# Performance work log

Hardware: AMD Instinct MI355X
Metric: run time of the kernel (lower is better)

## Reference

```python
import jax, jax.numpy as jnp
import numpy as np
import math

D_MODEL = 2048
H = 16
Q_LORA = 1536
KV_LORA = 512
DN = 128   # qk_nope_head_dim
DR = 64    # qk_rope_head_dim
DV = 128   # v_head_dim
B, S = 2, 2048
EPS = 1e-5


def layernorm(x, g, b):
    mu = jnp.mean(x, axis=-1, keepdims=True)
    var = jnp.mean(jnp.square(x - mu), axis=-1, keepdims=True)
    return (x - mu) * jax.lax.rsqrt(var + EPS) * g + b


def rope_cos_sin(position_ids, dim):
    inv_freq = 1.0 / (10000.0 ** (jnp.arange(0, dim, 2, dtype=jnp.float32) / dim))
    ang = position_ids.astype(jnp.float32)[:, None] * inv_freq[None, :]  # [S, dim/2]
    return jnp.cos(ang), jnp.sin(ang)


def apply_rope(x, cos, sin):
    # x: [..., S, ..., dim]; cos/sin broadcastable [..., S, ..., dim/2]
    x1, x2 = jnp.split(x, 2, axis=-1)
    return jnp.concatenate([x1 * cos - x2 * sin, x1 * sin + x2 * cos], axis=-1)


def setup_inputs() -> dict:
    key = jax.random.key(0)
    ks = jax.random.split(key, 8)
    sc = 0.02
    return {
        "hidden_states": jax.random.normal(ks[0], (B, S, D_MODEL), jnp.float32),
        "w_qa": jax.random.normal(ks[1], (Q_LORA, D_MODEL), jnp.float32) * sc,
        "ln_qa_g": jnp.ones((Q_LORA,), jnp.float32),
        "ln_qa_b": jnp.zeros((Q_LORA,), jnp.float32),
        "w_qb": jax.random.normal(ks[2], (H * DN, Q_LORA), jnp.float32) * sc,
        "w_qrope": jax.random.normal(ks[3], (H * DR, Q_LORA), jnp.float32) * sc,
        "w_kva": jax.random.normal(ks[4], (KV_LORA + DR, D_MODEL), jnp.float32) * sc,
        "ln_kva_g": jnp.ones((KV_LORA,), jnp.float32),
        "ln_kva_b": jnp.zeros((KV_LORA,), jnp.float32),
        "w_kvb": jax.random.normal(ks[5], (H * (DN + DV), KV_LORA), jnp.float32) * sc,
        "w_o": jax.random.normal(ks[6], (D_MODEL, H * DV), jnp.float32) * sc,
        "position_ids": jnp.arange(S, dtype=jnp.int32),
    }


def reference(hidden_states, w_qa, ln_qa_g, ln_qa_b, w_qb, w_qrope,
              w_kva, ln_kva_g, ln_kva_b, w_kvb, w_o, position_ids):
    bsz, seq_len, _ = hidden_states.shape

    # --- Q path (low-rank) ---
    q_latent = layernorm(hidden_states @ w_qa.T, ln_qa_g, ln_qa_b)        # [B,S,Q_LORA]
    q_nope = (q_latent @ w_qb.T).reshape(bsz, seq_len, H, DN)             # [B,S,H,DN]
    q_rope = (q_latent @ w_qrope.T).reshape(bsz, seq_len, H, DR)          # [B,S,H,DR]

    # --- absorb k up-projection into q ---
    k_up = w_kvb[: H * DN].reshape(H, DN, KV_LORA)
    v_up = w_kvb[H * DN:].reshape(H, DV, KV_LORA)
    q_abs = jnp.einsum('bshd,hdr->bshr', q_nope, k_up)                    # [B,S,H,R]

    # --- KV latent path ---
    kv_mixed = hidden_states @ w_kva.T                                    # [B,S,R+DR]
    kv_latent = layernorm(kv_mixed[..., :KV_LORA], ln_kva_g, ln_kva_b)    # [B,S,R]
    k_rope = kv_mixed[..., KV_LORA:]                                      # [B,S,DR]

    # --- RoPE ---
    cos, sin = rope_cos_sin(position_ids, DR)                             # [S,DR/2]
    q_rope = apply_rope(q_rope, cos[None, :, None, :], sin[None, :, None, :])
    k_rope = apply_rope(k_rope, cos[None, :, :], sin[None, :, :])

    # --- attention over latent channel (keys shared across heads) ---
    q_full = jnp.concatenate([q_abs, q_rope], axis=-1)                    # [B,S,H,R+DR]
    k_full = jnp.concatenate([kv_latent, k_rope], axis=-1)                # [B,S,R+DR]
    scale = 1.0 / math.sqrt(DN + DR)
    scores = jnp.einsum('bqhc,bkc->bhqk', q_full, k_full) * scale
    probs = jax.nn.softmax(scores, axis=-1)
    attn = jnp.einsum('bhqk,bkr->bhqr', probs, kv_latent)                 # [B,H,S,R]

    # --- absorbed v up-projection + output ---
    attn_v = jnp.einsum('bhqr,hvr->bqhv', attn, v_up)                     # [B,S,H,DV]
    attn_v = attn_v.reshape(bsz, seq_len, H * DV)
    return attn_v @ w_o.T                                                 # [B,S,D_MODEL]
```

## Files before the change

kernel.cpp:

```cpp
#include <hip/hip_runtime.h>
#include <math.h>

#define D_MODEL 2048
#define NH 16
#define Q_LORA 1536
#define KV_LORA 512
#define DN 128
#define DR 64
#define DV 128
#define BB 2
#define SS 2048
#define NROWS (BB*SS)
#define LN_EPS 1e-5f

typedef __attribute__((ext_vector_type(8))) short short8;
typedef __attribute__((ext_vector_type(4))) short short4v;
typedef __attribute__((ext_vector_type(4))) float f32x4;

__device__ __forceinline__ ushort f2bf(float f) {
    unsigned int u = __float_as_uint(f);
    u = u + 0x7fffu + ((u >> 16) & 1u);
    return (ushort)(u >> 16);
}

#if __has_builtin(__builtin_amdgcn_mfma_f32_16x16x16bf16_1k)
__device__ __forceinline__ f32x4 mfma16(short4v a, short4v b, f32x4 c) {
    return __builtin_amdgcn_mfma_f32_16x16x16bf16_1k(a, b, c, 0, 0, 0);
}
#elif __has_builtin(__builtin_amdgcn_mfma_f32_16x16x16_bf16)
__device__ __forceinline__ f32x4 mfma16(short4v a, short4v b, f32x4 c) {
    return __builtin_amdgcn_mfma_f32_16x16x16_bf16(a, b, c, 0, 0, 0);
}
#else
__device__ __forceinline__ f32x4 mfma16(short4v a, short4v b, f32x4 c) {
    asm volatile("v_mfma_f32_16x16x16_bf16 %0, %1, %2, %0"
                 : "+v"(c) : "v"(a), "v"(b));
    return c;
}
#endif

__device__ __forceinline__ void cv4(const float* __restrict__ s,
                                    ushort* __restrict__ d, long i) {
    float4 v = ((const float4*)s)[i];
    ushort4 o;
    o.x = f2bf(v.x); o.y = f2bf(v.y); o.z = f2bf(v.z); o.w = f2bf(v.w);
    ((ushort4*)d)[i] = o;
}

__global__ __launch_bounds__(256)
void cvt_all(const float* __restrict__ hs,     const float* __restrict__ w_qa,
             const float* __restrict__ w_qb,   const float* __restrict__ w_qrope,
             const float* __restrict__ w_kvb,  const float* __restrict__ w_kva,
             ushort* __restrict__ hs_bf,       ushort* __restrict__ w_qa_bf,
             ushort* __restrict__ w_qb_bf,     ushort* __restrict__ w_qrope_bf,
             ushort* __restrict__ w_kvb_bf,    ushort* __restrict__ w_kva_bf)
{
    long i = (long)blockIdx.x * 256 + threadIdx.x;
    if (i < 2097152) { cv4(hs, hs_bf, i); return; }
    i -= 2097152;
    if (i < 786432) { cv4(w_qa, w_qa_bf, i); return; }
    i -= 786432;
    if (i < 786432) { cv4(w_qb, w_qb_bf, i); return; }
    i -= 786432;
    if (i < 393216) { cv4(w_qrope, w_qrope_bf, i); return; }
    i -= 393216;
    if (i < 524288) { cv4(w_kvb, w_kvb_bf, i); return; }
    i -= 524288;
    if (i >= 327680) return;
    long e = i * 4;
    int row = (int)(e >> 11), col = (int)(e & 2047);
    ushort4 o;
    if (row < 576) {
        float4 v = *(const float4*)(w_kva + (long)row * 2048 + col);
        o.x = f2bf(v.x); o.y = f2bf(v.y); o.z = f2bf(v.z); o.w = f2bf(v.w);
    } else { o.x = 0; o.y = 0; o.z = 0; o.w = 0; }
    *(ushort4*)(w_kva_bf + (long)row * 2048 + col) = o;
}

__global__ __launch_bounds__(256)
void cvt_bf16(const float* __restrict__ in, ushort* __restrict__ out, long n4)
{
    long i = (long)blockIdx.x * 256 + threadIdx.x;
    if (i >= n4) return;
    cv4(in, out, i);
}

#define GLL16(g, l) \
    __builtin_amdgcn_global_load_lds((const __attribute__((address_space(1))) void*)(g), \
                                     (__attribute__((address_space(3))) void*)(l), 16, 0, 0)

__device__ __forceinline__ void gemm_core(const ushort* __restrict__ A,
    const ushort* __restrict__ Bp, ushort* As, ushort* Bs,
    int K, int lda, int ldb, int m0, int n0, int tid, f32x4 acc[4][4])
{
    int l = tid & 63, w = tid >> 6;
    int l15 = l & 15, quad = l >> 4;
    int wm = (w >> 1) * 64, wn = (w & 1) * 64;
    int ob = tid * 16;
    int row = ob >> 6, colb = ob & 63;
    const char* ga0 = (const char*)(A  + (long)(m0 + row) * lda)      + colb;
    const char* ga1 = (const char*)(A  + (long)(m0 + row + 64) * lda) + colb;
    const char* gb0 = (const char*)(Bp + (long)(n0 + row) * ldb)      + colb;
    const char* gb1 = (const char*)(Bp + (long)(n0 + row + 64) * ldb) + colb;
    ushort* la0 = As + tid * 8;
    ushort* la1 = As + 2048 + tid * 8;
    ushort* lb0 = Bs + tid * 8;
    ushort* lb1 = Bs + 2048 + tid * 8;

    for (int k0 = 0; k0 < K; k0 += 32) {
        GLL16(ga0, la0); GLL16(ga1, la1);
        GLL16(gb0, lb0); GLL16(gb1, lb1);
        ga0 += 64; ga1 += 64; gb0 += 64; gb1 += 64;
        __syncthreads();
        short8 af[4], bf[4];
        #pragma unroll
        for (int i = 0; i < 4; ++i)
            af[i] = *(const short8*)(As + (wm + i * 16 + l15) * 32 + quad * 8);
        #pragma unroll
        for (int j = 0; j < 4; ++j)
            bf[j] = *(const short8*)(Bs + (wn + j * 16 + l15) * 32 + quad * 8);
        #pragma unroll
        for (int i = 0; i < 4; ++i)
            #pragma unroll
            for (int j = 0; j < 4; ++j)
                acc[i][j] = __builtin_amdgcn_mfma_f32_16x16x32_bf16(
                    af[i], bf[j], acc[i][j], 0, 0, 0);
        __syncthreads();
    }
}

__global__ __launch_bounds__(256)
void gemm_f32out(const ushort* __restrict__ A, const ushort* __restrict__ B,
                 float* __restrict__ C, int K, int lda, int ldb, int ldc)
{
    __shared__ __align__(16) ushort As[128 * 32];
    __shared__ __align__(16) ushort Bs[128 * 32];
    int tid = threadIdx.x;
    int m0 = blockIdx.y * 128, n0 = blockIdx.x * 128;
    f32x4 acc[4][4] = {};
    gemm_core(A, B, As, Bs, K, lda, ldb, m0, n0, tid, acc);
    int l = tid & 63, w = tid >> 6;
    int l15 = l & 15, quad = l >> 4;
    int wm = (w >> 1) * 64, wn = (w & 1) * 64;
    #pragma unroll
    for (int i = 0; i < 4; ++i)
        #pragma unroll
        for (int j = 0; j < 4; ++j)
            #pragma unroll
            for (int r = 0; r < 4; ++r) {
                long gm = m0 + wm + i * 16 + quad * 4 + r;
                long gn = n0 + wn + j * 16 + l15;
                C[gm * ldc + gn] = acc[i][j][r];
            }
}

__global__ __launch_bounds__(256)
void gemm_dual(const ushort* __restrict__ A, const ushort* __restrict__ Bqa,
               const ushort* __restrict__ Bkva, float* __restrict__ Cq,
               float* __restrict__ Ckv)
{
    __shared__ __align__(16) ushort As[128 * 32];
    __shared__ __align__(16) ushort Bs[128 * 32];
    int tid = threadIdx.x;
    int bx = blockIdx.x;
    int m0 = blockIdx.y * 128;
    const ushort* Bp; float* C; int ldc, n0;
    if (bx < 12) { n0 = bx * 128;        Bp = Bqa  + (long)n0 * 2048; C = Cq;  ldc = 1536; }
    else         { n0 = (bx - 12) * 128; Bp = Bkva + (long)n0 * 2048; C = Ckv; ldc = 640; }
    f32x4 acc[4][4] = {};
    gemm_core(A, Bp, As, Bs, D_MODEL, D_MODEL, D_MODEL, m0, 0, tid, acc);
    int l = tid & 63, w = tid >> 6;
    int l15 = l & 15, quad = l >> 4;
    int wm = (w >> 1) * 64, wn = (w & 1) * 64;
    #pragma unroll
    for (int i = 0; i < 4; ++i)
        #pragma unroll
        for (int j = 0; j < 4; ++j)
            #pragma unroll
            for (int r = 0; r < 4; ++r) {
                long gm = m0 + wm + i * 16 + quad * 4 + r;
                long gn = n0 + wn + j * 16 + l15;
                C[gm * ldc + gn] = acc[i][j][r];
            }
}

__global__ __launch_bounds__(256)
void gemm_q23(const ushort* __restrict__ A, const ushort* __restrict__ Bqb,
              const ushort* __restrict__ Bqr, ushort* __restrict__ qfull,
              const float2* __restrict__ tab)
{
    __shared__ __align__(16) ushort As[128 * 32];
    __shared__ __align__(16) ushort Bs[128 * 32];
    int tid = threadIdx.x;
    int m0 = blockIdx.y * 128, n0 = blockIdx.x * 128;
    const ushort* Bp = (n0 < 2048) ? Bqb + (long)n0 * Q_LORA
                                   : Bqr + (long)(n0 - 2048) * Q_LORA;
    f32x4 acc[4][4] = {};
    gemm_core(A, Bp, As, Bs, Q_LORA, Q_LORA, Q_LORA, m0, 0, tid, acc);
    int l = tid & 63, w = tid >> 6;
    int l15 = l & 15, quad = l >> 4;
    int wm = (w >> 1) * 64, wn = (w & 1) * 64;
    if (n0 < 2048) {
        int head = n0 >> 7;
        #pragma unroll
        for (int i = 0; i < 4; ++i)
            #pragma unroll
            for (int j = 0; j < 4; ++j)
                #pragma unroll
                for (int r = 0; r < 4; ++r) {
                    long gm = m0 + wm + i * 16 + quad * 4 + r;
                    int c = wn + j * 16 + l15;
                    qfull[(gm * NH + head) * 192 + c] = f2bf(acc[i][j][r]);
                }
    } else {
        int nb = n0 - 2048;
        int head = (nb + wn) >> 6;
        #pragma unroll
        for (int i = 0; i < 4; ++i)
            #pragma unroll
            for (int j = 0; j < 2; ++j)
                #pragma unroll
                for (int r = 0; r < 4; ++r) {
                    long gm = m0 + wm + i * 16 + quad * 4 + r;
                    int ir = j * 16 + l15;
                    int s = (int)(gm & (SS - 1));
                    float2 cs = tab[s * 32 + ir];
                    float x1 = acc[i][j][r], x2 = acc[i][j + 2][r];
                    ushort* op = qfull + (gm * NH + head) * 192 + 128;
                    op[ir]      = f2bf(x1 * cs.x - x2 * cs.y);
                    op[ir + 32] = f2bf(x1 * cs.y + x2 * cs.x);
                }
    }
}

__global__ __launch_bounds__(256)
void gemm_kv56(const ushort* __restrict__ A, const ushort* __restrict__ B,
               ushort* __restrict__ kfull, ushort* __restrict__ vt)
{
    __shared__ __align__(16) ushort As[128 * 32];
    __shared__ __align__(16) ushort Bs[128 * 32];
    int tid = threadIdx.x;
    int m0 = blockIdx.y * 128, n0 = blockIdx.x * 128;
    const ushort* Bp = B + (long)n0 * KV_LORA;
    f32x4 acc[4][4] = {};
    gemm_core(A, Bp, As, Bs, KV_LORA, KV_LORA, KV_LORA, m0, 0, tid, acc);
    int l = tid & 63, w = tid >> 6;
    int l15 = l & 15, quad = l >> 4;
    int wm = (w >> 1) * 64, wn = (w & 1) * 64;
    if (n0 < 2048) {
        int head = n0 >> 7;
        #pragma unroll
        for (int i = 0; i < 4; ++i)
            #pragma unroll
            for (int j = 0; j < 4; ++j)
                #pragma unroll
                for (int r = 0; r < 4; ++r) {
                    long gm = m0 + wm + i * 16 + quad * 4 + r;
                    int c = wn + j * 16 + l15;
                    kfull[(gm * NH + head) * 192 + c] = f2bf(acc[i][j][r]);
                }
    } else {
        int head = (n0 >> 7) - 16;
        #pragma unroll
        for (int i = 0; i < 4; ++i)
            #pragma unroll
            for (int j = 0; j < 4; ++j) {
                long gm0 = m0 + wm + i * 16 + quad * 4;
                int c = wn + j * 16 + l15;
                ushort4 p;
                p.x = f2bf(acc[i][j][0]); p.y = f2bf(acc[i][j][1]);
                p.z = f2bf(acc[i][j][2]); p.w = f2bf(acc[i][j][3]);
                *(ushort4*)(vt + (long)head * 128 * 4096 + (long)c * 4096 + gm0) = p;
            }
    }
}

__global__ __launch_bounds__(256)
void ln_rows_bf(const float* __restrict__ in, ushort* __restrict__ out,
                const float* __restrict__ g, const float* __restrict__ b,
                int n, int ld_in, int ld_out)
{
    long rowi = blockIdx.x;
    const float* x = in + rowi * ld_in;
    ushort* y = out + rowi * ld_out;
    int tid = threadIdx.x;
    float s = 0.f, ss = 0.f;
    for (int i = tid; i < n; i += 256) { float v = x[i]; s += v; ss += v * v; }
    #pragma unroll
    for (int off = 32; off > 0; off >>= 1) {
        s  += __shfl_xor(s, off);
        ss += __shfl_xor(ss, off);
    }
    __shared__ float sred[4], ssred[4];
    int wid = tid >> 6, lane = tid & 63;
    if (lane == 0) { sred[wid] = s; ssred[wid] = ss; }
    __syncthreads();
    s  = sred[0] + sred[1] + sred[2] + sred[3];
    ss = ssred[0] + ssred[1] + ssred[2] + ssred[3];
    float mu  = s / n;
    float var = ss / n - mu * mu;
    float r = 1.0f / sqrtf(var + LN_EPS);
    for (int i = tid; i < n; i += 256)
        y[i] = f2bf((x[i] - mu) * r * g[i] + b[i]);
}

__global__ __launch_bounds__(256)
void rope_tab_k(const int* __restrict__ pos, float2* __restrict__ tab)
{
    int idx = blockIdx.x * 256 + threadIdx.x;
    if (idx >= SS * 32) return;
    int i = idx & 31;
    int s = idx >> 5;
    double ang = (double)pos[s] * exp(-(double)i * 0.28782313662425572);
    float2 cs;
    cs.x = (float)cos(ang);
    cs.y = (float)sin(ang);
    tab[idx] = cs;
}

__global__ __launch_bounds__(256)
void rope_k(const float* __restrict__ kvm, ushort* __restrict__ kfull,
            const float2* __restrict__ tab)
{
    long idx = (long)blockIdx.x * 256 + threadIdx.x;
    if (idx >= (long)NROWS * 32) return;
    int i = (int)(idx & 31);
    long rowi = idx >> 5;
    int s = (int)(rowi & (SS - 1));
    float2 cs = tab[s * 32 + i];
    float c = cs.x, sn = cs.y;
    const float* p = kvm + rowi * 640 + 512;
    float x1 = p[i], x2 = p[i + 32];
    ushort v1 = f2bf(x1 * c - x2 * sn);
    ushort v2 = f2bf(x1 * sn + x2 * c);
    ushort* o = kfull + rowi * NH * 192 + 128;
    #pragma unroll
    for (int h = 0; h < NH; ++h) {
        o[h * 192 + i]      = v1;
        o[h * 192 + i + 32] = v2;
    }
}

#define FSCALE 0.07216878364870322f

__global__ __launch_bounds__(512, 4)
void flash_mfma(const ushort* __restrict__ qf, const ushort* __restrict__ kf,
                const ushort* __restrict__ vt, ushort* __restrict__ attnv)
{
    __shared__ __align__(16) ushort Ks[64 * 192];
    __shared__ __align__(16) ushort Vs[128 * 64];
    int tid = threadIdx.x;
    int w = tid >> 6, l = tid & 63, l15 = l & 15, quad = l >> 4;
    int bh = blockIdx.x;
    int b = bh >> 4, h = bh & 15;
    int q0 = blockIdx.y * 128;

    const ushort* qp = qf + ((long)(b * SS + q0 + 16 * w + l15) * NH + h) * 192 + quad * 8;
    short8 aq[6];
    #pragma unroll
    for (int kk = 0; kk < 6; ++kk) aq[kk] = *(const short8*)(qp + kk * 32);

    f32x4 o[8] = {};
    float lsum = 0.f;
    float mrow = -INFINITY;

    const ushort* kbase = kf + ((long)(b * SS) * NH + h) * 192;
    const ushort* vbase = vt + (long)h * 128 * 4096 + (long)b * SS;

    int r0k = tid >> 3, subk = tid & 7;
    int v0  = tid >> 2, subv = tid & 3;
    const ushort* kgp = kbase + (long)r0k * (NH * 192);
    const ushort* vgp = vbase + (long)v0 * 4096;

    short8 pk[3], pv[2];
    #pragma unroll
    for (int it = 0; it < 3; ++it)
        pk[it] = *(const short8*)(kgp + (subk + 8 * it) * 8);
    #pragma unroll
    for (int it = 0; it < 2; ++it)
        pv[it] = *(const short8*)(vgp + (subv + 4 * it) * 8);

    int ksw = r0k & 7, vsw = v0 & 7;

    for (int k0 = 0; k0 < SS; k0 += 64) {
        __syncthreads();
        #pragma unroll
        for (int it = 0; it < 3; ++it)
            *(short8*)&Ks[r0k * 192 + ((subk + 8 * it) ^ ksw) * 8] = pk[it];
        #pragma unroll
        for (int it = 0; it < 2; ++it)
            *(short8*)&Vs[v0 * 64 + ((subv + 4 * it) ^ vsw) * 8] = pv[it];
        __syncthreads();
        if (k0 + 64 < SS) {
            const ushort* kg = kgp + (long)(k0 + 64) * (NH * 192);
            const ushort* vg = vgp + (k0 + 64);
            #pragma unroll
            for (int it = 0; it < 3; ++it)
                pk[it] = *(const short8*)(kg + (subk + 8 * it) * 8);
            #pragma unroll
            for (int it = 0; it < 2; ++it)
                pv[it] = *(const short8*)(vg + (subv + 4 * it) * 8);
        }

        f32x4 sc[4] = {};
        #pragma unroll
        for (int kk = 0; kk < 6; ++kk) {
            #pragma unroll
            for (int j = 0; j < 4; ++j) {
                int krow = j * 16 + l15;
                short8 kfr = *(const short8*)&Ks[krow * 192 + (((kk * 4 + quad) ^ (krow & 7))) * 8];
                sc[j] = __builtin_amdgcn_mfma_f32_16x16x32_bf16(kfr, aq[kk], sc[j], 0, 0, 0);
            }
        }

        float rmax = fmaxf(
            fmaxf(fmaxf(fmaxf(sc[0][0], sc[0][1]), fmaxf(sc[0][2], sc[0][3])),
                  fmaxf(fmaxf(sc[1][0], sc[1][1]), fmaxf(sc[1][2], sc[1][3]))),
            fmaxf(fmaxf(fmaxf(sc[2][0], sc[2][1]), fmaxf(sc[2][2], sc[2][3])),
                  fmaxf(fmaxf(sc[3][0], sc[3][1]), fmaxf(sc[3][2], sc[3][3]))));
        rmax = fmaxf(rmax, __shfl_xor(rmax, 16));
        rmax = fmaxf(rmax, __shfl_xor(rmax, 32));
        float pmax = rmax * FSCALE;

        if (__any(pmax > mrow + 8.0f)) {
            float mnew = fmaxf(mrow, pmax);
            float alpha = __expf(mrow - mnew);
            mrow = mnew;
            lsum *= alpha;
            float a0 = __shfl(alpha, quad * 4 + 0);
            float a1 = __shfl(alpha, quad * 4 + 1);
            float a2 = __shfl(alpha, quad * 4 + 2);
            float a3 = __shfl(alpha, quad * 4 + 3);
            #pragma unroll
            for (int v8 = 0; v8 < 8; ++v8) {
                o[v8][0] *= a0; o[v8][1] *= a1;
                o[v8][2] *= a2; o[v8][3] *= a3;
            }
        }

        float tsum = 0.f;
        #pragma unroll
        for (int j = 0; j < 4; ++j) {
            float p0 = __expf(fmaf(sc[j][0], FSCALE, -mrow));
            float p1 = __expf(fmaf(sc[j][1], FSCALE, -mrow));
            float p2 = __expf(fmaf(sc[j][2], FSCALE, -mrow));
            float p3 = __expf(fmaf(sc[j][3], FSCALE, -mrow));
            tsum += (p0 + p1) + (p2 + p3);
            short4v pf;
            pf[0] = (short)f2bf(p0); pf[1] = (short)f2bf(p1);
            pf[2] = (short)f2bf(p2); pf[3] = (short)f2bf(p3);
            #pragma unroll
            for (int v8 = 0; v8 < 8; ++v8) {
                int vrow = v8 * 16 + l15;
                int chunk = (2 * j + (quad >> 1)) ^ (vrow & 7);
                short4v bv = *(const short4v*)&Vs[vrow * 64 + chunk * 8 + 4 * (quad & 1)];
                o[v8] = mfma16(pf, bv, o[v8]);
            }
        }
        tsum += __shfl_xor(tsum, 16);
        tsum += __shfl_xor(tsum, 32);
        lsum += tsum;
    }

    #pragma unroll
    for (int r = 0; r < 4; ++r) {
        float Lq = __shfl(lsum, quad * 4 + r);
        float inv = 1.0f / Lq;
        long rowi = (long)(b * SS) + q0 + 16 * w + quad * 4 + r;
        ushort* op = attnv + (rowi * NH + h) * 128;
        #pragma unroll
        for (int v8 = 0; v8 < 8; ++v8)
            op[v8 * 16 + l15] = f2bf(o[v8][r] * inv);
    }
}


extern "C" void kernel_launch(void* const* d_in, const int* in_sizes, int n_in,
                              void* d_out, int out_size, void* d_ws, size_t ws_size,
                              hipStream_t stream) {
    const float* hs       = (const float*)d_in[0];
    const float* w_qa     = (const float*)d_in[1];
    const float* ln_qa_g  = (const float*)d_in[2];
    const float* ln_qa_b  = (const float*)d_in[3];
    const float* w_qb     = (const float*)d_in[4];
    const float* w_qrope  = (const float*)d_in[5];
    const float* w_kva    = (const float*)d_in[6];
    const float* ln_kva_g = (const float*)d_in[7];
    const float* ln_kva_b = (const float*)d_in[8];
    const float* w_kvb    = (const float*)d_in[9];
    const float* w_o      = (const float*)d_in[10];
    const int*   pos      = (const int*)d_in[11];
    float* out = (float*)d_out;

    char* W = (char*)d_ws;
    ushort* hs_bf     = (ushort*)(W + 0);
    ushort* w_o_bf    = (ushort*)(W + 0);
    ushort* w_qa_bf   = (ushort*)(W + 16777216);
    ushort* w_qb_bf   = (ushort*)(W + 23068672);
    ushort* w_qrope_bf= (ushort*)(W + 29360128);
    ushort* w_kva_bf  = (ushort*)(W + 32505856);
    ushort* w_kvb_bf  = (ushort*)(W + 35127296);
    float*  q_lat_f   = (float*)(W + 39321600);
    ushort* q_lat_bf  = (ushort*)(W + 64487424);
    float*  kv_mix    = (float*)(W + 77070336);
    ushort* kv_lat_bf = (ushort*)(W + 87556096);
    ushort* q_full    = (ushort*)(W + 91750400);
    ushort* k_full    = (ushort*)(W + 116916224);
    ushort* v_exp_t   = (ushort*)(W + 142082048);
    ushort* attnv_bf  = (ushort*)(W + 158859264);
    float2* rope_tab  = (float2*)(W + 158859264);

    dim3 blk(256);

    rope_tab_k<<<dim3(256), blk, 0, stream>>>(pos, rope_tab);
    cvt_all<<<dim3(19200), blk, 0, stream>>>(
        hs, w_qa, w_qb, w_qrope, w_kvb, w_kva,
        hs_bf, w_qa_bf, w_qb_bf, w_qrope_bf, w_kvb_bf, w_kva_bf);
    gemm_dual<<<dim3(17, 32), blk, 0, stream>>>(
        hs_bf, w_qa_bf, w_kva_bf, q_lat_f, kv_mix);
    cvt_bf16<<<dim3(4096), blk, 0, stream>>>(w_o, w_o_bf, 1048576);
    ln_rows_bf<<<dim3(NROWS), blk, 0, stream>>>(
        q_lat_f, q_lat_bf, ln_qa_g, ln_qa_b, Q_LORA, Q_LORA, Q_LORA);
    ln_rows_bf<<<dim3(NROWS), blk, 0, stream>>>(
        kv_mix, kv_lat_bf, ln_kva_g, ln_kva_b, KV_LORA, 640, KV_LORA);
    rope_k<<<dim3(512), blk, 0, stream>>>(kv_mix, k_full, rope_tab);
    gemm_q23<<<dim3(24, 32), blk, 0, stream>>>(
        q_lat_bf, w_qb_bf, w_qrope_bf, q_full, rope_tab);
    gemm_kv56<<<dim3(32, 32), blk, 0, stream>>>(
        kv_lat_bf, w_kvb_bf, k_full, v_exp_t);
    flash_mfma<<<dim3(BB * NH, SS / 128), dim3(512), 0, stream>>>(
        q_full, k_full, v_exp_t, attnv_bf);
    gemm_f32out<<<dim3(16, 32), blk, 0, stream>>>(
        attnv_bf, w_o_bf, out, NH * DV, NH * DV, NH * DV, D_MODEL);
}
```

Baseline: 529.8 us.

## Use 16x16x32 MFMA for PV via LDS-staged P and MFMA-computed row sums

Probabilities are now written to an LDS buffer and reread in the A-operand layout, so the PV product uses 16x16x32 bf16 MFMAs instead of 16x16x16. The softmax denominator comes from an extra MFMA against a block of ones appended to the V tile, which drops the per-tile shuffle reductions and summation. s_setprio brackets around the MFMA sections are meant to favour matrix issue. In exchange each tile adds LDS traffic for P, uses more shared memory, and computes the row sum from bf16-rounded probabilities.

```diff
diff --git a/kernel.cpp b/kernel.cpp
--- a/kernel.cpp
+++ b/kernel.cpp
@@ -14,7 +14,6 @@
 #define LN_EPS 1e-5f
 
 typedef __attribute__((ext_vector_type(8))) short short8;
-typedef __attribute__((ext_vector_type(4))) short short4v;
 typedef __attribute__((ext_vector_type(4))) float f32x4;
 
 __device__ __forceinline__ ushort f2bf(float f) {
@@ -22,22 +21,6 @@
     u = u + 0x7fffu + ((u >> 16) & 1u);
     return (ushort)(u >> 16);
 }
-
-#if __has_builtin(__builtin_amdgcn_mfma_f32_16x16x16bf16_1k)
-__device__ __forceinline__ f32x4 mfma16(short4v a, short4v b, f32x4 c) {
-    return __builtin_amdgcn_mfma_f32_16x16x16bf16_1k(a, b, c, 0, 0, 0);
-}
-#elif __has_builtin(__builtin_amdgcn_mfma_f32_16x16x16_bf16)
-__device__ __forceinline__ f32x4 mfma16(short4v a, short4v b, f32x4 c) {
-    return __builtin_amdgcn_mfma_f32_16x16x16_bf16(a, b, c, 0, 0, 0);
-}
-#else
-__device__ __forceinline__ f32x4 mfma16(short4v a, short4v b, f32x4 c) {
-    asm volatile("v_mfma_f32_16x16x16_bf16 %0, %1, %2, %0"
-                 : "+v"(c) : "v"(a), "v"(b));
-    return c;
-}
-#endif
 
 __device__ __forceinline__ void cv4(const float* __restrict__ s,
                                     ushort* __restrict__ d, long i) {
@@ -348,20 +331,29 @@
                 const ushort* __restrict__ vt, ushort* __restrict__ attnv)
 {
     __shared__ __align__(16) ushort Ks[64 * 192];
-    __shared__ __align__(16) ushort Vs[128 * 64];
+    __shared__ __align__(16) ushort Vs[144 * 64];
+    __shared__ __align__(16) ushort Ps[128 * 72];
     int tid = threadIdx.x;
     int w = tid >> 6, l = tid & 63, l15 = l & 15, quad = l >> 4;
     int bh = blockIdx.x;
     int b = bh >> 4, h = bh & 15;
     int q0 = blockIdx.y * 128;
 
+    {
+        int e = 8192 + tid * 2;
+        ushort2 iv;
+        iv.x = (e     < 8256) ? (ushort)0x3F80 : (ushort)0;
+        iv.y = (e + 1 < 8256) ? (ushort)0x3F80 : (ushort)0;
+        *(ushort2*)&Vs[e] = iv;
+    }
+
     const ushort* qp = qf + ((long)(b * SS + q0 + 16 * w + l15) * NH + h) * 192 + quad * 8;
     short8 aq[6];
     #pragma unroll
     for (int kk = 0; kk < 6; ++kk) aq[kk] = *(const short8*)(qp + kk * 32);
 
     f32x4 o[8] = {};
-    float lsum = 0.f;
+    f32x4 osum = {};
     float mrow = -INFINITY;
 
     const ushort* kbase = kf + ((long)(b * SS) * NH + h) * 192;
@@ -403,6 +395,7 @@
         }
 
         f32x4 sc[4] = {};
+        __builtin_amdgcn_s_setprio(1);
         #pragma unroll
         for (int kk = 0; kk < 6; ++kk) {
             #pragma unroll
@@ -412,6 +405,7 @@
                 sc[j] = __builtin_amdgcn_mfma_f32_16x16x32_bf16(kfr, aq[kk], sc[j], 0, 0, 0);
             }
         }
+        __builtin_amdgcn_s_setprio(0);
 
         float rmax = fmaxf(
             fmaxf(fmaxf(fmaxf(sc[0][0], sc[0][1]), fmaxf(sc[0][2], sc[0][3])),
@@ -426,7 +420,6 @@
             float mnew = fmaxf(mrow, pmax);
             float alpha = __expf(mrow - mnew);
             mrow = mnew;
-            lsum *= alpha;
             float a0 = __shfl(alpha, quad * 4 + 0);
             float a1 = __shfl(alpha, quad * 4 + 1);
             float a2 = __shfl(alpha, quad * 4 + 2);
@@ -436,36 +429,45 @@
                 o[v8][0] *= a0; o[v8][1] *= a1;
                 o[v8][2] *= a2; o[v8][3] *= a3;
             }
+            osum[0] *= a0; osum[1] *= a1; osum[2] *= a2; osum[3] *= a3;
         }
 
-        float tsum = 0.f;
+        int prow = (16 * w + l15) * 72 + quad * 4;
         #pragma unroll
         for (int j = 0; j < 4; ++j) {
             float p0 = __expf(fmaf(sc[j][0], FSCALE, -mrow));
             float p1 = __expf(fmaf(sc[j][1], FSCALE, -mrow));
             float p2 = __expf(fmaf(sc[j][2], FSCALE, -mrow));
             float p3 = __expf(fmaf(sc[j][3], FSCALE, -mrow));
-            tsum += (p0 + p1) + (p2 + p3);
-            short4v pf;
-            pf[0] = (short)f2bf(p0); pf[1] = (short)f2bf(p1);
-            pf[2] = (short)f2bf(p2); pf[3] = (short)f2bf(p3);
+            uint2 pu;
+            pu.x = (uint)f2bf(p0) | ((uint)f2bf(p1) << 16);
+            pu.y = (uint)f2bf(p2) | ((uint)f2bf(p3) << 16);
+            *(uint2*)&Ps[prow + j * 16] = pu;
+        }
+
+        __builtin_amdgcn_s_setprio(1);
+        #pragma unroll
+        for (int ks = 0; ks < 2; ++ks) {
+            short8 pa = *(const short8*)&Ps[(16 * w + l15) * 72 + ks * 32 + quad * 8];
             #pragma unroll
             for (int v8 = 0; v8 < 8; ++v8) {
                 int vrow = v8 * 16 + l15;
-                int chunk = (2 * j + (quad >> 1)) ^ (vrow & 7);
-                short4v bv = *(const short4v*)&Vs[vrow * 64 + chunk * 8 + 4 * (quad & 1)];
-                o[v8] = mfma16(pf, bv, o[v8]);
+                short8 bv = *(const short8*)&Vs[vrow * 64 + (((ks * 4 + quad) ^ (vrow & 7))) * 8];
+                o[v8] = __builtin_amdgcn_mfma_f32_16x16x32_bf16(pa, bv, o[v8], 0, 0, 0);
+            }
+            {
+                int vrow = 128 + l15;
+                short8 bv = *(const short8*)&Vs[vrow * 64 + (((ks * 4 + quad) ^ (vrow & 7))) * 8];
+                osum = __builtin_amdgcn_mfma_f32_16x16x32_bf16(pa, bv, osum, 0, 0, 0);
             }
         }
-        tsum += __shfl_xor(tsum, 16);
-        tsum += __shfl_xor(tsum, 32);
-        lsum += tsum;
+        __builtin_amdgcn_s_setprio(0);
     }
 
     #pragma unroll
     for (int r = 0; r < 4; ++r) {
-        float Lq = __shfl(lsum, quad * 4 + r);
-        float inv = 1.0f / Lq;
+        float lsum = __shfl(osum[r], l & 48);
+        float inv = 1.0f / lsum;
         long rowi = (long)(b * SS) + q0 + 16 * w + quad * 4 + r;
         ushort* op = attnv + (rowi * NH + h) * 128;
         #pragma unroll
```

Result: faster. 519.3 us (-2.0%).
